# Kernel optimization log

Hardware: AMD Instinct MI355X
Metric: run time of the kernel (lower is better)

Reference implementation:

```python
import jax, jax.numpy as jnp
import numpy as np


def reference(key, value, time_decay, time_first):
    # key, value: [B, T, H]; time_decay/time_first: [H]
    u = time_first
    w = -jnp.exp(time_decay)
    B, T, H = key.shape

    def step(carry, kv):
        a, b, exponent = carry  # each [B, H]
        kt, vt = kv             # [B, H] each
        # numerically stabilized WKV output at this timestep
        max_e = jnp.maximum(exponent, u + kt)
        wt = jnp.exp(u + kt - max_e)
        scale = jnp.exp(exponent - max_e)
        wkv = (a * scale + wt * vt) / (b * scale + wt)
        # state update with decay w
        max_e2 = jnp.maximum(exponent + w, kt)
        s1 = jnp.exp(exponent + w - max_e2)
        s2 = jnp.exp(kt - max_e2)
        a_new = s1 * a + s2 * vt
        b_new = s1 * b + s2
        return (a_new, b_new, max_e2), wkv

    init = (
        jnp.zeros((B, H), dtype=key.dtype),
        jnp.zeros((B, H), dtype=key.dtype),
        jnp.full((B, H), -jnp.inf, dtype=key.dtype),
    )
    k_t = jnp.transpose(key, (1, 0, 2))    # [T, B, H]
    v_t = jnp.transpose(value, (1, 0, 2))  # [T, B, H]
    _, out = jax.lax.scan(step, init, (k_t, v_t))
    return jnp.transpose(out, (1, 0, 2))   # [B, T, H]


def setup_inputs() -> dict:
    k = jax.random.key(0)
    k1, k2, k3, k4 = jax.random.split(k, 4)
    B, T, H = 8, 2048, 768
    return {
        "key": jax.random.normal(k1, (B, T, H), dtype=jnp.float32),
        "value": jax.random.normal(k2, (B, T, H), dtype=jnp.float32),
        "time_decay": jax.random.normal(k3, (H,), dtype=jnp.float32),
        "time_first": jax.random.normal(k4, (H,), dtype=jnp.float32),
    }
```

## Files before the change

### kernel.cpp

```cpp
#include <hip/hip_runtime.h>
#include <math.h>


#define B_  8
#define T_  2048
#define H_  768
#define NC_ 32
#define L_  64

__global__ __launch_bounds__(256) void wkv_phase1(
    const float* __restrict__ key, const float* __restrict__ val,
    const float* __restrict__ time_decay,
    float* __restrict__ wa, float* __restrict__ wb, float* __restrict__ we)
{
    const int h = blockIdx.x * 256 + threadIdx.x;
    const int c = blockIdx.y;
    const int b = blockIdx.z;

    const float w = -__expf(time_decay[h]);

    const size_t base = ((size_t)b * T_ + (size_t)c * L_) * H_ + h;
    const float* kp = key + base;
    const float* vp = val + base;

    float a = 0.f, bb = 0.f, e = -INFINITY;
#pragma unroll 4
    for (int t = 0; t < L_; ++t) {
        const float kt = kp[(size_t)t * H_];
        const float vt = vp[(size_t)t * H_];
        const float ew = e + w;
        const float m2 = fmaxf(ew, kt);
        const float s1 = __expf(ew - m2);
        const float s2 = __expf(kt - m2);
        a  = fmaf(s1, a,  s2 * vt);
        bb = fmaf(s1, bb, s2);
        e  = m2;
    }
    const size_t off = ((size_t)b * NC_ + c) * H_ + h;
    wa[off] = a; wb[off] = bb; we[off] = e;
}

__global__ __launch_bounds__(256) void wkv_phase2(
    float* __restrict__ wa, float* __restrict__ wb, float* __restrict__ we,
    const float* __restrict__ time_decay)
{
    const int idx = blockIdx.x * 256 + threadIdx.x;
    const int b = idx / H_;
    const int h = idx - b * H_;

    const float wL = -__expf(time_decay[h]) * (float)L_;

    float ra = 0.f, rb = 0.f, re = -INFINITY;

    size_t off = (size_t)b * NC_ * H_ + h;
    float ca = wa[off], cb = wb[off], ce = we[off];

#pragma unroll
    for (int c = 0; c < NC_; ++c) {
        const size_t noff = off + H_;
        float na = 0.f, nb = 0.f, ne = 0.f;
        if (c + 1 < NC_) {
            na = wa[noff]; nb = wb[noff]; ne = we[noff];
        }
        wa[off] = ra; wb[off] = rb; we[off] = re;

        const float e1 = re + wL;
        const float m  = fmaxf(e1, ce);
        const float p  = __expf(e1 - m);
        const float q  = __expf(ce - m);
        ra = fmaf(ra, p, ca * q);
        rb = fmaf(rb, p, cb * q);
        re = m;

        ca = na; cb = nb; ce = ne;
        off = noff;
    }
}

__global__ __launch_bounds__(256) void wkv_phase3(
    const float* __restrict__ key, const float* __restrict__ val,
    const float* __restrict__ time_decay, const float* __restrict__ time_first,
    const float* __restrict__ wa, const float* __restrict__ wb,
    const float* __restrict__ we, float* __restrict__ out)
{
    const int h = blockIdx.x * 256 + threadIdx.x;
    const int c = blockIdx.y;
    const int b = blockIdx.z;

    const float u = time_first[h];
    const float w = -__expf(time_decay[h]);

    const size_t soff = ((size_t)b * NC_ + c) * H_ + h;
    float a  = wa[soff];
    float bb = wb[soff];
    float e  = we[soff];

    const size_t base = ((size_t)b * T_ + (size_t)c * L_) * H_ + h;
    const float* kp = key + base;
    const float* vp = val + base;
    float*       op = out + base;

#pragma unroll 4
    for (int t = 0; t < L_; ++t) {
        const float kt = kp[(size_t)t * H_];
        const float vt = vp[(size_t)t * H_];

        const float uk = u + kt;
        const float m1 = fmaxf(e, uk);
        const float wt = __expf(uk - m1);
        const float sc = __expf(e - m1);
        const float num = fmaf(a,  sc, wt * vt);
        const float den = fmaf(bb, sc, wt);
        op[(size_t)t * H_] = num / den;

        const float ew = e + w;
        const float m2 = fmaxf(ew, kt);
        const float s1 = __expf(ew - m2);
        const float s2 = __expf(kt - m2);
        a  = fmaf(s1, a,  s2 * vt);
        bb = fmaf(s1, bb, s2);
        e  = m2;
    }
}

extern "C" void kernel_launch(void* const* d_in, const int* in_sizes, int n_in,
                              void* d_out, int out_size, void* d_ws, size_t ws_size,
                              hipStream_t stream) {
    const float* key = (const float*)d_in[0];
    const float* val = (const float*)d_in[1];
    const float* td  = (const float*)d_in[2];
    const float* tf  = (const float*)d_in[3];
    float* out = (float*)d_out;

    float* wa = (float*)d_ws;
    float* wb = wa + (size_t)B_ * NC_ * H_;
    float* we = wb + (size_t)B_ * NC_ * H_;

    dim3 blk(256);
    dim3 grid13(H_ / 256, NC_, B_);
    wkv_phase1<<<grid13, blk, 0, stream>>>(key, val, td, wa, wb, we);

    dim3 grid2((B_ * H_) / 256);
    wkv_phase2<<<grid2, blk, 0, stream>>>(wa, wb, we, td);

    wkv_phase3<<<grid13, blk, 0, stream>>>(key, val, td, tf, wa, wb, we, out);
}
```

Baseline: 162.9 us.

## Vectorize WKV chunk kernels with float4, pack state, pick chunk count by workspace

Each thread in phases 1 and 3 now handles four adjacent channels using float4 loads and stores, with a one-step software prefetch of the next key/value row. The three state arrays are packed into one float4 workspace, and the chunk count is a template parameter chosen from the available workspace size (up to 128 chunks), which gives shorter serial chains and more blocks. Phase 2 uses a prefetch ring, and the division is replaced by a hardware reciprocal that is less exact. The packed state spends an extra unused float per entry, and more chunks make the serial phase-2 scan longer.

Measured after the change: 176.7 us. 8.5% more time.

```diff
diff --git a/kernel.cpp b/kernel.cpp
--- a/kernel.cpp
+++ b/kernel.cpp
@@ -2,125 +2,169 @@
 #include <math.h>
 
 
-#define B_  8
-#define T_  2048
-#define H_  768
-#define NC_ 32
-#define L_  64
+#define B_   8
+#define T_   2048
+#define H_   768
+#define TPB_ 192
 
-__global__ __launch_bounds__(256) void wkv_phase1(
+__device__ __forceinline__ float rcp_f(float x) { return __builtin_amdgcn_rcpf(x); }
+
+template <int NC>
+__global__ __launch_bounds__(TPB_) void wkv_phase1(
     const float* __restrict__ key, const float* __restrict__ val,
-    const float* __restrict__ time_decay,
-    float* __restrict__ wa, float* __restrict__ wb, float* __restrict__ we)
+    const float* __restrict__ time_decay, float4* __restrict__ ws)
 {
-    const int h = blockIdx.x * 256 + threadIdx.x;
-    const int c = blockIdx.y;
-    const int b = blockIdx.z;
+    constexpr int L = T_ / NC;
+    const int h0 = threadIdx.x * 4;
+    const int c = blockIdx.x, b = blockIdx.y;
 
-    const float w = -__expf(time_decay[h]);
+    const float4 td = *(const float4*)(time_decay + h0);
+    const float w[4] = { -__expf(td.x), -__expf(td.y), -__expf(td.z), -__expf(td.w) };
 
-    const size_t base = ((size_t)b * T_ + (size_t)c * L_) * H_ + h;
-    const float* kp = key + base;
-    const float* vp = val + base;
+    const size_t base = ((size_t)b * T_ + (size_t)c * L) * (H_ / 4) + (h0 >> 2);
+    const float4* kp = (const float4*)key + base;
+    const float4* vp = (const float4*)val + base;
 
-    float a = 0.f, bb = 0.f, e = -INFINITY;
+    float a[4] = {0.f, 0.f, 0.f, 0.f};
+    float bb[4] = {0.f, 0.f, 0.f, 0.f};
+    float e[4] = {-INFINITY, -INFINITY, -INFINITY, -INFINITY};
+
+    float4 kt = kp[0], vt = vp[0];
 #pragma unroll 4
-    for (int t = 0; t < L_; ++t) {
-        const float kt = kp[(size_t)t * H_];
-        const float vt = vp[(size_t)t * H_];
-        const float ew = e + w;
-        const float m2 = fmaxf(ew, kt);
-        const float s1 = __expf(ew - m2);
-        const float s2 = __expf(kt - m2);
-        a  = fmaf(s1, a,  s2 * vt);
-        bb = fmaf(s1, bb, s2);
-        e  = m2;
+    for (int t = 0; t < L; ++t) {
+        float4 kn, vn;
+        if (t + 1 < L) {
+            kn = kp[(size_t)(t + 1) * (H_ / 4)];
+            vn = vp[(size_t)(t + 1) * (H_ / 4)];
+        }
+        const float kk[4] = {kt.x, kt.y, kt.z, kt.w};
+        const float vv[4] = {vt.x, vt.y, vt.z, vt.w};
+#pragma unroll
+        for (int j = 0; j < 4; ++j) {
+            const float ew = e[j] + w[j];
+            const float m2 = fmaxf(ew, kk[j]);
+            const float s1 = __expf(ew - m2);
+            const float s2 = __expf(kk[j] - m2);
+            a[j]  = fmaf(s1, a[j],  s2 * vv[j]);
+            bb[j] = fmaf(s1, bb[j], s2);
+            e[j]  = m2;
+        }
+        kt = kn; vt = vn;
     }
-    const size_t off = ((size_t)b * NC_ + c) * H_ + h;
-    wa[off] = a; wb[off] = bb; we[off] = e;
+
+    const size_t off = ((size_t)b * NC + c) * H_ + h0;
+#pragma unroll
+    for (int j = 0; j < 4; ++j)
+        ws[off + j] = make_float4(a[j], bb[j], e[j], 0.f);
 }
 
+template <int NC, int P>
 __global__ __launch_bounds__(256) void wkv_phase2(
-    float* __restrict__ wa, float* __restrict__ wb, float* __restrict__ we,
-    const float* __restrict__ time_decay)
+    float4* __restrict__ ws, const float* __restrict__ time_decay)
 {
+    constexpr int L = T_ / NC;
     const int idx = blockIdx.x * 256 + threadIdx.x;
     const int b = idx / H_;
     const int h = idx - b * H_;
 
-    const float wL = -__expf(time_decay[h]) * (float)L_;
+    const float wL = -__expf(time_decay[h]) * (float)L;
+
+    const size_t off0 = (size_t)b * NC * H_ + h;
+    float4 ring[P];
+#pragma unroll
+    for (int p = 0; p < P; ++p) ring[p] = ws[off0 + (size_t)p * H_];
 
     float ra = 0.f, rb = 0.f, re = -INFINITY;
-
-    size_t off = (size_t)b * NC_ * H_ + h;
-    float ca = wa[off], cb = wb[off], ce = we[off];
-
-#pragma unroll
-    for (int c = 0; c < NC_; ++c) {
-        const size_t noff = off + H_;
-        float na = 0.f, nb = 0.f, ne = 0.f;
-        if (c + 1 < NC_) {
-            na = wa[noff]; nb = wb[noff]; ne = we[noff];
-        }
-        wa[off] = ra; wb[off] = rb; we[off] = re;
+#pragma unroll 8
+    for (int c = 0; c < NC; ++c) {
+        const float4 cur = ring[c & (P - 1)];
+        if (c + P < NC) ring[c & (P - 1)] = ws[off0 + (size_t)(c + P) * H_];
+        ws[off0 + (size_t)c * H_] = make_float4(ra, rb, re, 0.f);
 
         const float e1 = re + wL;
-        const float m  = fmaxf(e1, ce);
-        const float p  = __expf(e1 - m);
-        const float q  = __expf(ce - m);
-        ra = fmaf(ra, p, ca * q);
-        rb = fmaf(rb, p, cb * q);
+        const float m  = fmaxf(e1, cur.z);
+        const float p_ = __expf(e1 - m);
+        const float q_ = __expf(cur.z - m);
+        ra = fmaf(ra, p_, cur.x * q_);
+        rb = fmaf(rb, p_, cur.y * q_);
         re = m;
-
-        ca = na; cb = nb; ce = ne;
-        off = noff;
     }
 }
 
-__global__ __launch_bounds__(256) void wkv_phase3(
+template <int NC>
+__global__ __launch_bounds__(TPB_) void wkv_phase3(
     const float* __restrict__ key, const float* __restrict__ val,
     const float* __restrict__ time_decay, const float* __restrict__ time_first,
-    const float* __restrict__ wa, const float* __restrict__ wb,
-    const float* __restrict__ we, float* __restrict__ out)
+    const float4* __restrict__ ws, float* __restrict__ out)
 {
-    const int h = blockIdx.x * 256 + threadIdx.x;
-    const int c = blockIdx.y;
-    const int b = blockIdx.z;
+    constexpr int L = T_ / NC;
+    const int h0 = threadIdx.x * 4;
+    const int c = blockIdx.x, b = blockIdx.y;
 
-    const float u = time_first[h];
-    const float w = -__expf(time_decay[h]);
+    const float4 td = *(const float4*)(time_decay + h0);
+    const float4 tf = *(const float4*)(time_first + h0);
+    const float w[4] = { -__expf(td.x), -__expf(td.y), -__expf(td.z), -__expf(td.w) };
+    const float u[4] = { tf.x, tf.y, tf.z, tf.w };
 
-    const size_t soff = ((size_t)b * NC_ + c) * H_ + h;
-    float a  = wa[soff];
-    float bb = wb[soff];
-    float e  = we[soff];
+    const size_t soff = ((size_t)b * NC + c) * H_ + h0;
+    float a[4], bb[4], e[4];
+#pragma unroll
+    for (int j = 0; j < 4; ++j) {
+        const float4 s = ws[soff + j];
+        a[j] = s.x; bb[j] = s.y; e[j] = s.z;
+    }
 
-    const size_t base = ((size_t)b * T_ + (size_t)c * L_) * H_ + h;
-    const float* kp = key + base;
-    const float* vp = val + base;
-    float*       op = out + base;
+    const size_t base = ((size_t)b * T_ + (size_t)c * L) * (H_ / 4) + (h0 >> 2);
+    const float4* kp = (const float4*)key + base;
+    const float4* vp = (const float4*)val + base;
+    float4*       op = (float4*)out + base;
 
+    float4 kt = kp[0], vt = vp[0];
 #pragma unroll 4
-    for (int t = 0; t < L_; ++t) {
-        const float kt = kp[(size_t)t * H_];
-        const float vt = vp[(size_t)t * H_];
+    for (int t = 0; t < L; ++t) {
+        float4 kn, vn;
+        if (t + 1 < L) {
+            kn = kp[(size_t)(t + 1) * (H_ / 4)];
+            vn = vp[(size_t)(t + 1) * (H_ / 4)];
+        }
+        const float kk[4] = {kt.x, kt.y, kt.z, kt.w};
+        const float vv[4] = {vt.x, vt.y, vt.z, vt.w};
+        float o[4];
+#pragma unroll
+        for (int j = 0; j < 4; ++j) {
+            const float uk = u[j] + kk[j];
+            const float m1 = fmaxf(e[j], uk);
+            const float wt = __expf(uk - m1);
+            const float sc = __expf(e[j] - m1);
+            const float num = fmaf(a[j],  sc, wt * vv[j]);
+            const float den = fmaf(bb[j], sc, wt);
+            o[j] = num * rcp_f(den);
 
-        const float uk = u + kt;
-        const float m1 = fmaxf(e, uk);
-        const float wt = __expf(uk - m1);
-        const float sc = __expf(e - m1);
-        const float num = fmaf(a,  sc, wt * vt);
-        const float den = fmaf(bb, sc, wt);
-        op[(size_t)t * H_] = num / den;
+            const float ew = e[j] + w[j];
+            const float m2 = fmaxf(ew, kk[j]);
+            const float s1 = __expf(ew - m2);
+            const float s2 = __expf(kk[j] - m2);
+            a[j]  = fmaf(s1, a[j],  s2 * vv[j]);
+            bb[j] = fmaf(s1, bb[j], s2);
+            e[j]  = m2;
+        }
+        op[(size_t)t * (H_ / 4)] = make_float4(o[0], o[1], o[2], o[3]);
+        kt = kn; vt = vn;
+    }
+}
 
-        const float ew = e + w;
-        const float m2 = fmaxf(ew, kt);
-        const float s1 = __expf(ew - m2);
-        const float s2 = __expf(kt - m2);
-        a  = fmaf(s1, a,  s2 * vt);
-        bb = fmaf(s1, bb, s2);
-        e  = m2;
-    }
+template <int NC>
+static void launch_all(const float* key, const float* val, const float* td,
+                       const float* tf, float* out, float4* ws, hipStream_t stream)
+{
+    dim3 blk13(TPB_);
+    dim3 grid13(NC, B_);
+    wkv_phase1<NC><<<grid13, blk13, 0, stream>>>(key, val, td, ws);
+
+    dim3 grid2((B_ * H_) / 256);
+    wkv_phase2<NC, 8><<<grid2, dim3(256), 0, stream>>>(ws, td);
+
+    wkv_phase3<NC><<<grid13, blk13, 0, stream>>>(key, val, td, tf, ws, out);
 }
 
 extern "C" void kernel_launch(void* const* d_in, const int* in_sizes, int n_in,
@@ -131,17 +175,14 @@
     const float* td  = (const float*)d_in[2];
     const float* tf  = (const float*)d_in[3];
     float* out = (float*)d_out;
+    float4* ws = (float4*)d_ws;
 
-    float* wa = (float*)d_ws;
-    float* wb = wa + (size_t)B_ * NC_ * H_;
-    float* we = wb + (size_t)B_ * NC_ * H_;
+    const size_t need128 = (size_t)B_ * 128 * H_ * sizeof(float4);
+    const size_t need64  = (size_t)B_ * 64  * H_ * sizeof(float4);
+    const size_t need32  = (size_t)B_ * 32  * H_ * sizeof(float4);
 
-    dim3 blk(256);
-    dim3 grid13(H_ / 256, NC_, B_);
-    wkv_phase1<<<grid13, blk, 0, stream>>>(key, val, td, wa, wb, we);
-
-    dim3 grid2((B_ * H_) / 256);
-    wkv_phase2<<<grid2, blk, 0, stream>>>(wa, wb, we, td);
-
-    wkv_phase3<<<grid13, blk, 0, stream>>>(key, val, td, tf, wa, wb, we, out);
+    if (ws_size >= need128)      launch_all<128>(key, val, td, tf, out, ws, stream);
+    else if (ws_size >= need64)  launch_all<64>(key, val, td, tf, out, ws, stream);
+    else if (ws_size >= need32)  launch_all<32>(key, val, td, tf, out, ws, stream);
+    else                         launch_all<16>(key, val, td, tf, out, ws, stream);
 }
```

## Template chunk count, add register prefetch, out-of-place chunk scan, fast reciprocal

Applied to the files above, without the earlier changes.

Makes the chunk count a template parameter and picks the largest one (up to 128) that fits in the workspace. More chunks means more parallel blocks and shorter sequential chains in phases 1 and 3. Both phases now prefetch k and v through a 4-deep register ring, and phase 3 replaces the division with a hardware reciprocal. Phase 2 batch-loads 8 chunk aggregates and writes prefix states to a separate buffer. The costs are a longer serial phase 2, a larger workspace, and slightly less precise division.

Result: slower. 169.0 us (+3.7%).

```diff
diff --git a/kernel.cpp b/kernel.cpp
--- a/kernel.cpp
+++ b/kernel.cpp
@@ -2,32 +2,45 @@
 #include <math.h>
 
 
-#define B_  8
-#define T_  2048
-#define H_  768
-#define NC_ 32
-#define L_  64
+#define B_   8
+#define T_   2048
+#define H_   768
 
+__device__ __forceinline__ float rcp_f(float x) { return __builtin_amdgcn_rcpf(x); }
+
+template <int NC>
 __global__ __launch_bounds__(256) void wkv_phase1(
     const float* __restrict__ key, const float* __restrict__ val,
     const float* __restrict__ time_decay,
-    float* __restrict__ wa, float* __restrict__ wb, float* __restrict__ we)
+    float* __restrict__ aggA, float* __restrict__ aggB, float* __restrict__ aggE)
 {
+    constexpr int L = T_ / NC;
+    constexpr int D = 4;
     const int h = blockIdx.x * 256 + threadIdx.x;
-    const int c = blockIdx.y;
-    const int b = blockIdx.z;
+    const int c = blockIdx.y, b = blockIdx.z;
 
     const float w = -__expf(time_decay[h]);
 
-    const size_t base = ((size_t)b * T_ + (size_t)c * L_) * H_ + h;
+    const size_t base = ((size_t)b * T_ + (size_t)c * L) * H_ + h;
     const float* kp = key + base;
     const float* vp = val + base;
 
+    float kbuf[D], vbuf[D];
+#pragma unroll
+    for (int i = 0; i < D; ++i) {
+        kbuf[i] = kp[(size_t)i * H_];
+        vbuf[i] = vp[(size_t)i * H_];
+    }
+
     float a = 0.f, bb = 0.f, e = -INFINITY;
-#pragma unroll 4
-    for (int t = 0; t < L_; ++t) {
-        const float kt = kp[(size_t)t * H_];
-        const float vt = vp[(size_t)t * H_];
+#pragma unroll
+    for (int t = 0; t < L; ++t) {
+        const float kt = kbuf[t & (D - 1)];
+        const float vt = vbuf[t & (D - 1)];
+        if (t + D < L) {
+            kbuf[t & (D - 1)] = kp[(size_t)(t + D) * H_];
+            vbuf[t & (D - 1)] = vp[(size_t)(t + D) * H_];
+        }
         const float ew = e + w;
         const float m2 = fmaxf(ew, kt);
         const float s1 = __expf(ew - m2);
@@ -36,74 +49,95 @@
         bb = fmaf(s1, bb, s2);
         e  = m2;
     }
-    const size_t off = ((size_t)b * NC_ + c) * H_ + h;
-    wa[off] = a; wb[off] = bb; we[off] = e;
+
+    const size_t off = ((size_t)b * NC + c) * H_ + h;
+    aggA[off] = a; aggB[off] = bb; aggE[off] = e;
 }
 
+template <int NC, int P>
 __global__ __launch_bounds__(256) void wkv_phase2(
-    float* __restrict__ wa, float* __restrict__ wb, float* __restrict__ we,
+    const float* __restrict__ aggA, const float* __restrict__ aggB,
+    const float* __restrict__ aggE,
+    float* __restrict__ stA, float* __restrict__ stB, float* __restrict__ stE,
     const float* __restrict__ time_decay)
 {
+    constexpr int L = T_ / NC;
     const int idx = blockIdx.x * 256 + threadIdx.x;
     const int b = idx / H_;
     const int h = idx - b * H_;
 
-    const float wL = -__expf(time_decay[h]) * (float)L_;
+    const float wL = -__expf(time_decay[h]) * (float)L;
+
+    const size_t off0 = (size_t)b * NC * H_ + h;
+    float ca[P], cb[P], ce[P];
+#pragma unroll
+    for (int p = 0; p < P; ++p) {
+        const size_t o = off0 + (size_t)p * H_;
+        ca[p] = aggA[o]; cb[p] = aggB[o]; ce[p] = aggE[o];
+    }
 
     float ra = 0.f, rb = 0.f, re = -INFINITY;
-
-    size_t off = (size_t)b * NC_ * H_ + h;
-    float ca = wa[off], cb = wb[off], ce = we[off];
-
 #pragma unroll
-    for (int c = 0; c < NC_; ++c) {
-        const size_t noff = off + H_;
-        float na = 0.f, nb = 0.f, ne = 0.f;
-        if (c + 1 < NC_) {
-            na = wa[noff]; nb = wb[noff]; ne = we[noff];
+    for (int c = 0; c < NC; ++c) {
+        const int s = c & (P - 1);
+        const float xa = ca[s], xb = cb[s], xe = ce[s];
+        if (c + P < NC) {
+            const size_t noff = off0 + (size_t)(c + P) * H_;
+            ca[s] = aggA[noff]; cb[s] = aggB[noff]; ce[s] = aggE[noff];
         }
-        wa[off] = ra; wb[off] = rb; we[off] = re;
+        const size_t coff = off0 + (size_t)c * H_;
+        stA[coff] = ra; stB[coff] = rb; stE[coff] = re;
 
         const float e1 = re + wL;
-        const float m  = fmaxf(e1, ce);
-        const float p  = __expf(e1 - m);
-        const float q  = __expf(ce - m);
-        ra = fmaf(ra, p, ca * q);
-        rb = fmaf(rb, p, cb * q);
+        const float m  = fmaxf(e1, xe);
+        const float p_ = __expf(e1 - m);
+        const float q_ = __expf(xe - m);
+        ra = fmaf(ra, p_, xa * q_);
+        rb = fmaf(rb, p_, xb * q_);
         re = m;
-
-        ca = na; cb = nb; ce = ne;
-        off = noff;
     }
 }
 
+template <int NC>
 __global__ __launch_bounds__(256) void wkv_phase3(
     const float* __restrict__ key, const float* __restrict__ val,
     const float* __restrict__ time_decay, const float* __restrict__ time_first,
-    const float* __restrict__ wa, const float* __restrict__ wb,
-    const float* __restrict__ we, float* __restrict__ out)
+    const float* __restrict__ stA, const float* __restrict__ stB,
+    const float* __restrict__ stE, float* __restrict__ out)
 {
+    constexpr int L = T_ / NC;
+    constexpr int D = 4;
     const int h = blockIdx.x * 256 + threadIdx.x;
-    const int c = blockIdx.y;
-    const int b = blockIdx.z;
+    const int c = blockIdx.y, b = blockIdx.z;
 
     const float u = time_first[h];
     const float w = -__expf(time_decay[h]);
 
-    const size_t soff = ((size_t)b * NC_ + c) * H_ + h;
-    float a  = wa[soff];
-    float bb = wb[soff];
-    float e  = we[soff];
+    const size_t soff = ((size_t)b * NC + c) * H_ + h;
+    float a  = stA[soff];
+    float bb = stB[soff];
+    float e  = stE[soff];
 
-    const size_t base = ((size_t)b * T_ + (size_t)c * L_) * H_ + h;
+    const size_t base = ((size_t)b * T_ + (size_t)c * L) * H_ + h;
     const float* kp = key + base;
     const float* vp = val + base;
     float*       op = out + base;
 
-#pragma unroll 4
-    for (int t = 0; t < L_; ++t) {
-        const float kt = kp[(size_t)t * H_];
-        const float vt = vp[(size_t)t * H_];
+    float kbuf[D], vbuf[D];
+#pragma unroll
+    for (int i = 0; i < D; ++i) {
+        kbuf[i] = kp[(size_t)i * H_];
+        vbuf[i] = vp[(size_t)i * H_];
+    }
+
+#pragma unroll
+    for (int t = 0; t < L; ++t) {
+        const float kt = kbuf[t & (D - 1)];
+        const float vt = vbuf[t & (D - 1)];
+        if (t + D < L) {
+            kbuf[t & (D - 1)] = kp[(size_t)(t + D) * H_];
+            vbuf[t & (D - 1)] = vp[(size_t)(t + D) * H_];
+        }
 
         const float uk = u + kt;
         const float m1 = fmaxf(e, uk);
@@ -111,7 +145,7 @@
         const float sc = __expf(e - m1);
         const float num = fmaf(a,  sc, wt * vt);
         const float den = fmaf(bb, sc, wt);
-        op[(size_t)t * H_] = num / den;
+        op[(size_t)t * H_] = num * rcp_f(den);
 
         const float ew = e + w;
         const float m2 = fmaxf(ew, kt);
@@ -123,6 +157,27 @@
     }
 }
 
+template <int NC>
+static void launch_all(const float* key, const float* val, const float* td,
+                       const float* tf, float* out, float* ws, hipStream_t stream)
+{
+    const size_t n = (size_t)B_ * NC * H_;
+    float* aggA = ws;
+    float* aggB = aggA + n;
+    float* aggE = aggB + n;
+    float* stA  = aggE + n;
+    float* stB  = stA + n;
+    float* stE  = stB + n;
+
+    dim3 grid13(H_ / 256, NC, B_);
+    wkv_phase1<NC><<<grid13, dim3(256), 0, stream>>>(key, val, td, aggA, aggB, aggE);
+
+    dim3 grid2((B_ * H_) / 256);
+    wkv_phase2<NC, 8><<<grid2, dim3(256), 0, stream>>>(aggA, aggB, aggE, stA, stB, stE, td);
+
+    wkv_phase3<NC><<<grid13, dim3(256), 0, stream>>>(key, val, td, tf, stA, stB, stE, out);
+}
+
 extern "C" void kernel_launch(void* const* d_in, const int* in_sizes, int n_in,
                               void* d_out, int out_size, void* d_ws, size_t ws_size,
                               hipStream_t stream) {
@@ -131,17 +186,11 @@
     const float* td  = (const float*)d_in[2];
     const float* tf  = (const float*)d_in[3];
     float* out = (float*)d_out;
+    float* ws = (float*)d_ws;
 
-    float* wa = (float*)d_ws;
-    float* wb = wa + (size_t)B_ * NC_ * H_;
-    float* we = wb + (size_t)B_ * NC_ * H_;
-
-    dim3 blk(256);
-    dim3 grid13(H_ / 256, NC_, B_);
-    wkv_phase1<<<grid13, blk, 0, stream>>>(key, val, td, wa, wb, we);
-
-    dim3 grid2((B_ * H_) / 256);
-    wkv_phase2<<<grid2, blk, 0, stream>>>(wa, wb, we, td);
-
-    wkv_phase3<<<grid13, blk, 0, stream>>>(key, val, td, tf, wa, wb, we, out);
+    const size_t perNC = (size_t)6 * B_ * H_ * sizeof(float);
+    if (ws_size >= 128 * perNC)      launch_all<128>(key, val, td, tf, out, ws, stream);
+    else if (ws_size >= 64 * perNC)  launch_all<64>(key, val, td, tf, out, ws, stream);
+    else if (ws_size >= 32 * perNC)  launch_all<32>(key, val, td, tf, out, ws, stream);
+    else                             launch_all<16>(key, val, td, tf, out, ws, stream);
 }
```
